# Kernel optimization log

Measured on AMD Instinct MI355X. Metric: run time of the kernel, lower is better.

The kernel has to match this reference:

```python
import jax, jax.numpy as jnp
import numpy as np
from jax import lax

EPS = 1e-5
TAU = 2.0
THR = 1.0

@jax.custom_vjp
def spike_fn(x):
    # torch.heaviside(x, 1.0): 1 where x >= 0, else 0
    return (x >= 0).astype(x.dtype)

def _spike_fwd(x):
    return spike_fn(x), x

def _spike_bwd(x, g):
    alpha = 4.0
    s = jax.nn.sigmoid(alpha * x)
    return (g * (1.0 - s) * s * alpha,)

spike_fn.defvjp(_spike_fwd, _spike_bwd)

def lif(x):
    # sequential membrane recurrence over dim 0 (time)
    def step(v, xt):
        v = v + (xt - v) / TAU
        s = spike_fn(v - THR)
        v = (1.0 - lax.stop_gradient(s)) * v
        return v, s
    _, spikes = lax.scan(step, jnp.zeros_like(x[0]), x)
    return spikes

def bn(x, p):
    # eval-mode BatchNorm2d; p = [weight, bias, mean, var], each [C]
    w, b, m, v = p
    inv = w / jnp.sqrt(v + EPS)
    return (x - m[None, :, None, None]) * inv[None, :, None, None] + b[None, :, None, None]

def bn_and_pad(x, p):
    # BN then pad 1 pixel on all sides with the BN-of-zero value
    w, b, m, v = p
    y = bn(x, p)
    pad_val = b - m * w / jnp.sqrt(v + EPS)  # [C]
    y = jnp.pad(y, ((0, 0), (0, 0), (1, 1), (1, 1)))
    pv = pad_val[None, :, None]  # broadcasts over batch and spatial
    y = y.at[:, :, 0, :].set(pv)
    y = y.at[:, :, -1, :].set(pv)
    y = y.at[:, :, :, 0].set(pv)
    y = y.at[:, :, :, -1].set(pv)
    return y

def branch(x, w1, dw, pw, bn3):
    # RepConv: 1x1 -> BNAndPad(1) -> depthwise3x3(valid) -> 1x1 -> BN, then outer BN
    C = x.shape[1]
    y = jnp.einsum('oc,bchw->bohw', w1, x)
    y = bn_and_pad(y, bn3[0])
    y = lax.conv_general_dilated(y, dw[:, None, :, :], (1, 1), 'VALID',
                                 dimension_numbers=('NCHW', 'OIHW', 'NCHW'),
                                 feature_group_count=C)
    y = jnp.einsum('oc,bchw->bohw', pw, y)
    y = bn(y, bn3[1])
    y = bn(y, bn3[2])
    return y

def _to_heads(t, B, N, h, d):
    # [B,C,H,W] -> [B,h,N,d]
    return t.reshape(B, h * d, N).transpose(0, 2, 1).reshape(B, N, h, d).transpose(0, 2, 1, 3)

def forward(x, q_w1, q_dw, q_pw, q_bn, k_w1, k_dw, k_pw, k_bn,
            v_w1, v_dw, v_pw, v_bn, p_w1, p_dw, p_pw, p_bn,
            num_heads=8):
    B, C, H, W = x.shape
    N = H * W
    h = num_heads
    d = C // h
    scale = float(d) ** -0.5

    xs = lif(x)
    q = lif(branch(xs, q_w1, q_dw, q_pw, q_bn))
    k = lif(branch(xs, k_w1, k_dw, k_pw, k_bn))
    v = lif(branch(xs, v_w1, v_dw, v_pw, v_bn))

    q = _to_heads(q, B, N, h, d)
    k = _to_heads(k, B, N, h, d)
    v = _to_heads(v, B, N, h, d)

    kv = jnp.einsum('bhnd,bhne->bhde', k, v)          # [B,h,d,d]
    o = jnp.einsum('bhnd,bhde->bhne', q, kv) * scale  # [B,h,N,d]
    o = o.transpose(0, 1, 3, 2).reshape(B, C, N)       # [B,C,N]
    o = lif(o)
    o = o.reshape(B, C, H, W)
    o = branch(o, p_w1, p_dw, p_pw, p_bn)
    return o.reshape(B, C, H, W)

def setup_inputs() -> dict:
    key = jax.random.key(0)
    ks = jax.random.split(key, 20)
    B, C, H, W = 8, 256, 64, 64
    s1 = 1.0 / np.sqrt(C)

    def make_bn(k):
        k1, k2, k3, k4 = jax.random.split(k, 4)
        w = 1.0 + 0.1 * jax.random.normal(k1, (3, C), jnp.float32)
        b = 0.1 * jax.random.normal(k2, (3, C), jnp.float32)
        m = 0.1 * jax.random.normal(k3, (3, C), jnp.float32)
        var = jax.random.uniform(k4, (3, C), jnp.float32, 0.5, 1.5)
        return jnp.stack([w, b, m, var], axis=1)  # [3,4,C]

    inp = {'x': jax.random.normal(ks[0], (B, C, H, W), jnp.float32)}
    for i, p in enumerate(['q', 'k', 'v', 'p']):
        kk = jax.random.split(ks[1 + i], 4)
        inp[p + '_w1'] = jax.random.normal(kk[0], (C, C), jnp.float32) * s1
        inp[p + '_dw'] = jax.random.normal(kk[1], (C, 3, 3), jnp.float32) * 0.3
        inp[p + '_pw'] = jax.random.normal(kk[2], (C, C), jnp.float32) * s1
        inp[p + '_bn'] = make_bn(kk[3])
    return inp

def reference(x, q_w1, q_dw, q_pw, q_bn, k_w1, k_dw, k_pw, k_bn,
              v_w1, v_dw, v_pw, v_bn, p_w1, p_dw, p_pw, p_bn):
    return forward(x, q_w1, q_dw, q_pw, q_bn, k_w1, k_dw, k_pw, k_bn,
                   v_w1, v_dw, v_pw, v_bn, p_w1, p_dw, p_pw, p_bn)
```

## Files before the change

### kernel.cpp

```cpp
#include <hip/hip_runtime.h>
#include <hip/hip_bf16.h>
#include <math.h>

#define T_ 8
#define C_ 256
#define N_ 4096
#define CN_ (C_ * N_)
#define EPSB 1e-5f

typedef unsigned long long u64;
typedef unsigned int u32;
typedef short bf16x8 __attribute__((ext_vector_type(8)));
typedef float f32x4 __attribute__((ext_vector_type(4)));

static __device__ __forceinline__ unsigned short f2bf(float f) {
    __hip_bfloat16 h = __float2bfloat16(f);
    return *(unsigned short*)&h;
}
static __device__ __forceinline__ float bf2f(unsigned short u) {
    u32 x = (u32)u << 16;
    return *(float*)&x;
}


__global__ __launch_bounds__(256) void lif_u8(const float* __restrict__ X,
                                              unsigned char* __restrict__ S) {
    int idx = blockIdx.x * 256 + threadIdx.x;
    float v = 0.f;
#pragma unroll
    for (int t = 0; t < T_; t++) {
        float xt = X[(size_t)t * CN_ + idx];
        v = v + (xt - v) / 2.0f;
        unsigned char s = (v - 1.0f >= 0.f) ? 1 : 0;
        S[(size_t)t * CN_ + idx] = s;
        if (s) v = 0.f;
    }
}

struct LArgs {
    const float* F[3];
    unsigned char* sq;
    u64* kbp;
    u64* vbp;
};
__global__ __launch_bounds__(256) void lif3(LArgs a) {
    int br = blockIdx.y;
    int idx = blockIdx.x * 256 + threadIdx.x;
    const float* X = a.F[br];
    int lane = threadIdx.x & 63;
    u64* BP = (br == 1) ? a.kbp : a.vbp;
    float v = 0.f;
#pragma unroll
    for (int t = 0; t < T_; t++) {
        float xt = X[(size_t)t * CN_ + idx];
        v = v + (xt - v) / 2.0f;
        int s = (v - 1.0f >= 0.f) ? 1 : 0;
        if (br == 0) {
            a.sq[(size_t)t * CN_ + idx] = (unsigned char)s;
        } else {
            u64 mask = __ballot(s);
            if (lane == 0) BP[((size_t)t * CN_ + idx) >> 6] = mask;
        }
        if (s) v = 0.f;
    }
}

struct WPtrs { const float* w[8]; };
__global__ __launch_bounds__(256) void split_w(WPtrs p, unsigned short* __restrict__ out) {
    int mat = blockIdx.y;
    int idx = blockIdx.x * 256 + threadIdx.x;
    int m = idx >> 8, k = idx & 255;
    float w = p.w[mat][idx];
    unsigned short h1 = f2bf(w);
    float f1 = bf2f(h1);
    unsigned short h2 = f2bf(w - f1);
    unsigned short h3 = f2bf(w - f1 - bf2f(h2));
    int lane = ((k >> 3) & 3) * 16 + (m & 15);
    size_t pos = ((size_t)(((m >> 4) * 8 + (k >> 5)) * 64 + lane)) * 8 + (k & 7);
    size_t base = (size_t)mat * 3 * 65536;
    out[base + pos] = h1;
    out[base + 65536 + pos] = h2;
    out[base + 2 * 65536 + pos] = h3;
}

__global__ __launch_bounds__(256) void trans_s(const unsigned char* __restrict__ S,
                                               unsigned short* __restrict__ ST) {
    int t = blockIdx.y;
    int nb = blockIdx.x * 32;
    const unsigned char* St = S + (size_t)t * CN_;
    __shared__ u32 L[32][257];
    int tid = threadIdx.x;
    int nof = (tid & 7) * 4;
    int kbase = tid >> 3;
#pragma unroll
    for (int it = 0; it < 8; it++) {
        int k = kbase + it * 32;
        uchar4 sv = *(const uchar4*)&St[(size_t)k * N_ + nb + nof];
        L[nof + 0][k] = sv.x ? 0x3F80u : 0u;
        L[nof + 1][k] = sv.y ? 0x3F80u : 0u;
        L[nof + 2][k] = sv.z ? 0x3F80u : 0u;
        L[nof + 3][k] = sv.w ? 0x3F80u : 0u;
    }
    __syncthreads();
    int n = tid & 31, k32 = tid >> 5;
    int n16 = (nb + n) >> 4;
    int lrow = n & 15;
    unsigned short* outt = ST + (size_t)t * CN_;
#pragma unroll
    for (int quad = 0; quad < 4; quad++) {
        bf16x8 bs;
#pragma unroll
        for (int j = 0; j < 8; j++)
            bs[j] = (short)(L[n][k32 * 32 + quad * 8 + j] & 0xffffu);
        *(bf16x8*)&outt[((size_t)(n16 * 8 + k32)) * 512 + (quad * 16 + lrow) * 8] = bs;
    }
}

static __device__ __forceinline__ void dw_body(const float* __restrict__ Yt,
                                               const float* __restrict__ dw,
                                               const float* __restrict__ bnp,
                                               unsigned short* __restrict__ Bh,
                                               unsigned short* __restrict__ Bl,
                                               int y0, int cg, int tid) {
    int c0 = cg * 8;
    __shared__ float L[8][6][68];
    __shared__ float invs[8], bs_[8], ms_[8], pads_[8];

    if (tid < 8) {
        int c = c0 + tid;
        float w = bnp[c], b = bnp[256 + c], m = bnp[512 + c], var = bnp[768 + c];
        float sq = sqrtf(var + EPSB);
        invs[tid] = w / sq;
        bs_[tid] = b;
        ms_[tid] = m;
        pads_[tid] = b - (m * w) / sq;
    }
    __syncthreads();

    for (int i = tid; i < 8 * 6 * 66; i += 256) {
        int c = i / 396;
        int rem = i - c * 396;
        int row = rem / 66, col = rem - row * 66;
        int gy = y0 - 1 + row, gx = col - 1;
        float val;
        if (gy < 0 || gy > 63 || gx < 0 || gx > 63) val = pads_[c];
        else val = (Yt[(size_t)(c0 + c) * N_ + gy * 64 + gx] - ms_[c]) * invs[c] + bs_[c];
        L[c][row][col] = val;
    }
    __syncthreads();

    int x = tid & 63, ry = tid >> 6;
    int n = (y0 + ry) * 64 + x;

    bf16x8 hi, lo;
#pragma unroll
    for (int j = 0; j < 8; j++) {
        const float* dwc = dw + (c0 + j) * 9;
        float a = 0.f;
#pragma unroll
        for (int dy = 0; dy < 3; dy++)
#pragma unroll
            for (int dx = 0; dx < 3; dx++)
                a += dwc[dy * 3 + dx] * L[j][ry + dy][x + dx];
        unsigned short h = f2bf(a);
        hi[j] = (short)h;
        lo[j] = (short)f2bf(a - bf2f(h));
    }
    size_t pos = ((size_t)((n >> 4) * 8 + (cg >> 2))) * 512 +
                 (size_t)(((cg & 3) * 16 + (n & 15)) * 8);
    *(bf16x8*)&Bh[pos] = hi;
    *(bf16x8*)&Bl[pos] = lo;
}

__global__ __launch_bounds__(256) void dw_bn_split(const float* __restrict__ Yin,
                                                   const float* __restrict__ dw,
                                                   const float* __restrict__ bnp,
                                                   unsigned short* __restrict__ BhT,
                                                   unsigned short* __restrict__ BlT) {
    int t = blockIdx.z;
    dw_body(Yin + (size_t)t * CN_, dw, bnp,
            BhT + (size_t)t * CN_, BlT + (size_t)t * CN_,
            blockIdx.x * 4, blockIdx.y, threadIdx.x);
}

struct DArgs {
    const float* F[3];
    const float* dw[3];
    const float* bn[3];
    unsigned short* Ph[3];
    unsigned short* Pl[3];
};
__global__ __launch_bounds__(256) void dw3(DArgs a) {
    int br = blockIdx.z >> 3, t = blockIdx.z & 7;
    dw_body(a.F[br] + (size_t)t * CN_, a.dw[br], a.bn[br],
            a.Ph[br] + (size_t)t * CN_, a.Pl[br] + (size_t)t * CN_,
            blockIdx.x * 4, blockIdx.y, threadIdx.x);
}

static __device__ __forceinline__ void gemm_s_core(const unsigned short* __restrict__ Wsp,
                                                   const unsigned short* __restrict__ Bt,
                                                   float* __restrict__ Yt,
                                                   int bx, int by, int tid) {
    int l = tid & 63, wave = tid >> 6;
    int wm = wave >> 1, wn = wave & 1;
    int lcol = l & 15, quad = l >> 4;

    f32x4 acc[4][4];
#pragma unroll
    for (int i = 0; i < 4; i++)
#pragma unroll
        for (int j = 0; j < 4; j++) acc[i][j] = (f32x4){0.f, 0.f, 0.f, 0.f};

#pragma unroll 2
    for (int k32 = 0; k32 < 8; k32++) {
        bf16x8 bfr[4];
#pragma unroll
        for (int nt = 0; nt < 4; nt++)
            bfr[nt] = *(const bf16x8*)&Bt[((size_t)((bx * 8 + wn * 4 + nt) * 8 + k32)) * 512 + l * 8];
#pragma unroll
        for (int s = 0; s < 3; s++) {
            const unsigned short* Ws = Wsp + (size_t)s * 65536;
#pragma unroll
            for (int mt = 0; mt < 4; mt++) {
                bf16x8 afr = *(const bf16x8*)&Ws[((size_t)((by * 8 + wm * 4 + mt) * 8 + k32)) * 512 + l * 8];
#pragma unroll
                for (int nt = 0; nt < 4; nt++)
                    acc[mt][nt] = __builtin_amdgcn_mfma_f32_16x16x32_bf16(
                        afr, bfr[nt], acc[mt][nt], 0, 0, 0);
            }
        }
    }

    int m0 = by * 128, n0 = bx * 128;
#pragma unroll
    for (int mt = 0; mt < 4; mt++)
#pragma unroll
        for (int i = 0; i < 4; i++) {
            int row = m0 + wm * 64 + mt * 16 + quad * 4 + i;
            float* yr = &Yt[(size_t)row * N_ + n0 + wn * 64 + lcol];
#pragma unroll
            for (int nt = 0; nt < 4; nt++) yr[nt * 16] = acc[mt][nt][i];
        }
}

static __device__ __forceinline__ void gemm_f_core(const unsigned short* __restrict__ Wsp,
                                                   const unsigned short* __restrict__ Bht,
                                                   const unsigned short* __restrict__ Blt,
                                                   float* __restrict__ Yt,
                                                   const float* __restrict__ bnp,
                                                   int bx, int by, int tid) {
    int l = tid & 63, wave = tid >> 6;
    int wm = wave >> 1, wn = wave & 1;
    int lcol = l & 15, quad = l >> 4;

    f32x4 acc[4][4];
#pragma unroll
    for (int i = 0; i < 4; i++)
#pragma unroll
        for (int j = 0; j < 4; j++) acc[i][j] = (f32x4){0.f, 0.f, 0.f, 0.f};

#pragma unroll 2
    for (int k32 = 0; k32 < 8; k32++) {
        bf16x8 bh[4], bl[4];
#pragma unroll
        for (int nt = 0; nt < 4; nt++) {
            size_t bpos = ((size_t)((bx * 8 + wn * 4 + nt) * 8 + k32)) * 512 + l * 8;
            bh[nt] = *(const bf16x8*)&Bht[bpos];
            bl[nt] = *(const bf16x8*)&Blt[bpos];
        }
#pragma unroll
        for (int s = 0; s < 3; s++) {
            const unsigned short* Ws = Wsp + (size_t)s * 65536;
#pragma unroll
            for (int mt = 0; mt < 4; mt++) {
                bf16x8 afr = *(const bf16x8*)&Ws[((size_t)((by * 8 + wm * 4 + mt) * 8 + k32)) * 512 + l * 8];
#pragma unroll
                for (int nt = 0; nt < 4; nt++)
                    acc[mt][nt] = __builtin_amdgcn_mfma_f32_16x16x32_bf16(
                        afr, bh[nt], acc[mt][nt], 0, 0, 0);
                if (s < 2) {
#pragma unroll
                    for (int nt = 0; nt < 4; nt++)
                        acc[mt][nt] = __builtin_amdgcn_mfma_f32_16x16x32_bf16(
                            afr, bl[nt], acc[mt][nt], 0, 0, 0);
                }
            }
        }
    }

    int m0 = by * 128, n0 = bx * 128;
#pragma unroll
    for (int mt = 0; mt < 4; mt++)
#pragma unroll
        for (int i = 0; i < 4; i++) {
            int row = m0 + wm * 64 + mt * 16 + quad * 4 + i;
            float i1 = bnp[1024 + row] / sqrtf(bnp[1024 + 768 + row] + EPSB);
            float b1 = bnp[1024 + 256 + row], m1 = bnp[1024 + 512 + row];
            float i2 = bnp[2048 + row] / sqrtf(bnp[2048 + 768 + row] + EPSB);
            float b2 = bnp[2048 + 256 + row], m2 = bnp[2048 + 512 + row];
            float* yr = &Yt[(size_t)row * N_ + n0 + wn * 64 + lcol];
#pragma unroll
            for (int nt = 0; nt < 4; nt++)
                yr[nt * 16] = ((acc[mt][nt][i] - m1) * i1 + b1 - m2) * i2 + b2;
        }
}

__global__ __launch_bounds__(256) void gemm_s2(const unsigned short* __restrict__ Wsp,
                                               const unsigned short* __restrict__ ST,
                                               float* __restrict__ Y) {
    int t = blockIdx.z;
    gemm_s_core(Wsp, ST + (size_t)t * CN_, Y + (size_t)t * CN_,
                blockIdx.x, blockIdx.y, threadIdx.x);
}
__global__ __launch_bounds__(256) void gemm_f2(const unsigned short* __restrict__ Wsp,
                                               const unsigned short* __restrict__ BhT,
                                               const unsigned short* __restrict__ BlT,
                                               float* __restrict__ Y,
                                               const float* __restrict__ bnp) {
    int t = blockIdx.z;
    gemm_f_core(Wsp, BhT + (size_t)t * CN_, BlT + (size_t)t * CN_,
                Y + (size_t)t * CN_, bnp, blockIdx.x, blockIdx.y, threadIdx.x);
}

struct GSArgs { const unsigned short* W[3]; const unsigned short* ST; float* F[3]; };
__global__ __launch_bounds__(256) void gemm_s3(GSArgs a) {
    int t = blockIdx.z;
    int br = blockIdx.y >> 1, byl = blockIdx.y & 1;
    gemm_s_core(a.W[br], a.ST + (size_t)t * CN_, a.F[br] + (size_t)t * CN_,
                blockIdx.x, byl, threadIdx.x);
}
struct GFArgs {
    const unsigned short* W[3];
    const unsigned short* Ph[3];
    const unsigned short* Pl[3];
    float* F[3];
    const float* bn[3];
};
__global__ __launch_bounds__(256) void gemm_f3(GFArgs a) {
    int t = blockIdx.z;
    int br = blockIdx.y >> 1, byl = blockIdx.y & 1;
    gemm_f_core(a.W[br], a.Ph[br] + (size_t)t * CN_, a.Pl[br] + (size_t)t * CN_,
                a.F[br] + (size_t)t * CN_, a.bn[br], blockIdx.x, byl, threadIdx.x);
}

__global__ __launch_bounds__(1024) void attn_kv_bp(const u64* __restrict__ Kbp,
                                                   const u64* __restrict__ Vbp,
                                                   float* __restrict__ kvbuf) {
    int th = blockIdx.x;
    int t = th >> 3, h = th & 7;
    const u64* kb = Kbp + ((size_t)t * C_ + h * 32) * 64;
    const u64* vb = Vbp + ((size_t)t * C_ + h * 32) * 64;
    __shared__ u64 ks[32][65];
    __shared__ u64 vs[32][65];
    int tid = threadIdx.x;
    {
        int r = tid >> 5, w2 = (tid & 31) * 2;
        ks[r][w2] = kb[r * 64 + w2];     ks[r][w2 + 1] = kb[r * 64 + w2 + 1];
        vs[r][w2] = vb[r * 64 + w2];     vs[r][w2 + 1] = vb[r * 64 + w2 + 1];
    }
    __syncthreads();
    int d = tid >> 5, e = tid & 31;
    int cnt = 0;
#pragma unroll
    for (int w = 0; w < 64; w++)
        cnt += __popcll(ks[d][w] & vs[e][w]);
    kvbuf[(size_t)th * 1024 + d * 32 + e] = (float)cnt;
}

__global__ __launch_bounds__(256) void attn_o_u8(const unsigned char* __restrict__ q,
                                                 const float* __restrict__ kvbuf,
                                                 float* __restrict__ o) {
    int t = blockIdx.z, h = blockIdx.y;
    int n = blockIdx.x * 1024 + threadIdx.x * 4;
    __shared__ float kvs[1024];
    const float* kv = kvbuf + (size_t)(t * 8 + h) * 1024;
    for (int i = threadIdx.x; i < 1024; i += 256) kvs[i] = kv[i];
    __syncthreads();
    const unsigned char* qb = q + (size_t)t * CN_ + (size_t)h * 32 * N_ + n;
    float* ob = o + (size_t)t * CN_ + (size_t)h * 32 * N_ + n;
    const float scale = 0.17677669529663687f;
#pragma unroll
    for (int eg = 0; eg < 2; eg++) {
        float acc[16][4];
#pragma unroll
        for (int e = 0; e < 16; e++)
#pragma unroll
            for (int j = 0; j < 4; j++) acc[e][j] = 0.f;
        for (int d = 0; d < 32; d++) {
            uchar4 qu = *(const uchar4*)(&qb[(size_t)d * N_]);
            float4 qv = {(float)qu.x, (float)qu.y, (float)qu.z, (float)qu.w};
#pragma unroll
            for (int e = 0; e < 16; e++) {
                float kvv = kvs[d * 32 + eg * 16 + e];
                acc[e][0] += qv.x * kvv;
                acc[e][1] += qv.y * kvv;
                acc[e][2] += qv.z * kvv;
                acc[e][3] += qv.w * kvv;
            }
        }
#pragma unroll
        for (int e = 0; e < 16; e++) {
            float4 ov = {acc[e][0] * scale, acc[e][1] * scale,
                         acc[e][2] * scale, acc[e][3] * scale};
            *(float4*)(&ob[(size_t)(eg * 16 + e) * N_]) = ov;
        }
    }
}

extern "C" void kernel_launch(void* const* d_in, const int* in_sizes, int n_in,
                              void* d_out, int out_size, void* d_ws, size_t ws_size,
                              hipStream_t stream) {
    const float* x = (const float*)d_in[0];
    const float* q_w1 = (const float*)d_in[1];
    const float* q_dw = (const float*)d_in[2];
    const float* q_pw = (const float*)d_in[3];
    const float* q_bn = (const float*)d_in[4];
    const float* k_w1 = (const float*)d_in[5];
    const float* k_dw = (const float*)d_in[6];
    const float* k_pw = (const float*)d_in[7];
    const float* k_bn = (const float*)d_in[8];
    const float* v_w1 = (const float*)d_in[9];
    const float* v_dw = (const float*)d_in[10];
    const float* v_pw = (const float*)d_in[11];
    const float* v_bn = (const float*)d_in[12];
    const float* p_w1 = (const float*)d_in[13];
    const float* p_dw = (const float*)d_in[14];
    const float* p_pw = (const float*)d_in[15];
    const float* p_bn = (const float*)d_in[16];

    const size_t SZ = (size_t)T_ * CN_;
    float* out = (float*)d_out;
    float* F0 = (float*)d_ws;
    float* F1 = F0 + SZ;
    float* F2 = F1 + SZ;
    float* P0 = F2 + SZ;
    float* P1 = P0 + SZ;
    float* P2 = P1 + SZ;
    float* bufKV = P2 + SZ;
    unsigned char* xs = (unsigned char*)(bufKV + 65536);
    unsigned char* sq = xs + SZ;
    u64* kbp = (u64*)(sq + SZ);
    u64* vbp = kbp + (SZ >> 6);
    unsigned short* wspA = (unsigned short*)(vbp + (SZ >> 6));
    unsigned short* ST = wspA + 8 * 3 * 65536;

    unsigned short* P0h = (unsigned short*)P0; unsigned short* P0l = P0h + SZ;
    unsigned short* P1h = (unsigned short*)P1; unsigned short* P1l = P1h + SZ;
    unsigned short* P2h = (unsigned short*)P2; unsigned short* P2l = P2h + SZ;

    dim3 gLif(CN_ / 256), bLif(256);
    dim3 gTr(N_ / 32, T_), bTr(256);

    WPtrs wp;
    wp.w[0] = q_w1; wp.w[1] = q_pw; wp.w[2] = k_w1; wp.w[3] = k_pw;
    wp.w[4] = v_w1; wp.w[5] = v_pw; wp.w[6] = p_w1; wp.w[7] = p_pw;
    split_w<<<dim3(256, 8), dim3(256), 0, stream>>>(wp, wspA);
    const size_t WS3 = 3 * 65536;

    lif_u8<<<gLif, bLif, 0, stream>>>(x, xs);
    trans_s<<<gTr, bTr, 0, stream>>>(xs, ST);

    GSArgs gs;
    gs.W[0] = wspA + 0 * WS3; gs.W[1] = wspA + 2 * WS3; gs.W[2] = wspA + 4 * WS3;
    gs.ST = ST; gs.F[0] = F0; gs.F[1] = F1; gs.F[2] = F2;
    gemm_s3<<<dim3(N_ / 128, 6, T_), dim3(256), 0, stream>>>(gs);

    DArgs da;
    da.F[0] = F0; da.F[1] = F1; da.F[2] = F2;
    da.dw[0] = q_dw; da.dw[1] = k_dw; da.dw[2] = v_dw;
    da.bn[0] = q_bn; da.bn[1] = k_bn; da.bn[2] = v_bn;
    da.Ph[0] = P0h; da.Ph[1] = P1h; da.Ph[2] = P2h;
    da.Pl[0] = P0l; da.Pl[1] = P1l; da.Pl[2] = P2l;
    dw3<<<dim3(16, 32, 3 * T_), dim3(256), 0, stream>>>(da);

    GFArgs gf;
    gf.W[0] = wspA + 1 * WS3; gf.W[1] = wspA + 3 * WS3; gf.W[2] = wspA + 5 * WS3;
    gf.Ph[0] = P0h; gf.Ph[1] = P1h; gf.Ph[2] = P2h;
    gf.Pl[0] = P0l; gf.Pl[1] = P1l; gf.Pl[2] = P2l;
    gf.F[0] = F0; gf.F[1] = F1; gf.F[2] = F2;
    gf.bn[0] = q_bn; gf.bn[1] = k_bn; gf.bn[2] = v_bn;
    gemm_f3<<<dim3(N_ / 128, 6, T_), dim3(256), 0, stream>>>(gf);

    LArgs la;
    la.F[0] = F0; la.F[1] = F1; la.F[2] = F2;
    la.sq = sq; la.kbp = kbp; la.vbp = vbp;
    lif3<<<dim3(CN_ / 256, 3), dim3(256), 0, stream>>>(la);

    attn_kv_bp<<<dim3(64), dim3(1024), 0, stream>>>(kbp, vbp, bufKV);
    attn_o_u8<<<dim3(4, 8, 8), dim3(256), 0, stream>>>(sq, bufKV, F0);
    lif_u8<<<gLif, bLif, 0, stream>>>(F0, xs);
    trans_s<<<gTr, bTr, 0, stream>>>(xs, ST);

    gemm_s2<<<dim3(N_ / 128, C_ / 128, T_), dim3(256), 0, stream>>>(wspA + 6 * WS3, ST, out);
    dw_bn_split<<<dim3(16, 32, T_), dim3(256), 0, stream>>>(out, p_dw, p_bn, P0h, P0l);
    gemm_f2<<<dim3(N_ / 128, C_ / 128, T_), dim3(256), 0, stream>>>(wspA + 7 * WS3, P0h, P0l, out, p_bn);
}
```

Measured before the change: 442.7 us.

## Fuse LIF with spike transpose, and attention output with LIF

The input LIF now writes bf16 MFMA-fragment spikes directly, so the separate uint8 spike buffer and transpose kernel are gone. The attention-output kernel now loops over time per head, keeps membrane state in registers, and emits bf16 fragment spikes directly. This removes the fp32 attention-output buffer, the second LIF pass and a transpose, saving global memory traffic and several launches. In exchange the new kernels synchronise at every timestep, and attn_olif launches far fewer blocks and reads q with byte-sized loads, which may lower occupancy and memory efficiency.

```diff
diff --git a/kernel.cpp b/kernel.cpp
--- a/kernel.cpp
+++ b/kernel.cpp
@@ -23,17 +23,33 @@
 }
 
 
-__global__ __launch_bounds__(256) void lif_u8(const float* __restrict__ X,
-                                              unsigned char* __restrict__ S) {
-    int idx = blockIdx.x * 256 + threadIdx.x;
+__global__ __launch_bounds__(256) void lif_x_frag(const float* __restrict__ X,
+                                                  unsigned short* __restrict__ ST) {
+    int nb = blockIdx.x * 32;
+    int c0 = blockIdx.y * 8;
+    int tid = threadIdx.x;
+    int nj = tid & 31, ci = tid >> 5;
+    size_t base = (size_t)(c0 + ci) * N_ + nb + nj;
+    __shared__ unsigned short Ls[8][34];
+    int k32 = c0 >> 5, quad = (c0 >> 3) & 3;
     float v = 0.f;
 #pragma unroll
     for (int t = 0; t < T_; t++) {
-        float xt = X[(size_t)t * CN_ + idx];
+        float xt = X[(size_t)t * CN_ + base];
         v = v + (xt - v) / 2.0f;
-        unsigned char s = (v - 1.0f >= 0.f) ? 1 : 0;
-        S[(size_t)t * CN_ + idx] = s;
+        int s = (v - 1.0f >= 0.f) ? 1 : 0;
+        Ls[ci][nj] = s ? (unsigned short)0x3F80 : (unsigned short)0;
         if (s) v = 0.f;
+        __syncthreads();
+        if (tid < 32) {
+            int np = nb + tid;
+            bf16x8 bs;
+#pragma unroll
+            for (int j = 0; j < 8; j++) bs[j] = (short)Ls[j][tid];
+            *(bf16x8*)&ST[(size_t)t * CN_ +
+                ((size_t)((np >> 4) * 8 + k32)) * 512 + (quad * 16 + (np & 15)) * 8] = bs;
+        }
+        __syncthreads();
     }
 }
 
@@ -83,39 +99,6 @@
     out[base + 2 * 65536 + pos] = h3;
 }
 
-__global__ __launch_bounds__(256) void trans_s(const unsigned char* __restrict__ S,
-                                               unsigned short* __restrict__ ST) {
-    int t = blockIdx.y;
-    int nb = blockIdx.x * 32;
-    const unsigned char* St = S + (size_t)t * CN_;
-    __shared__ u32 L[32][257];
-    int tid = threadIdx.x;
-    int nof = (tid & 7) * 4;
-    int kbase = tid >> 3;
-#pragma unroll
-    for (int it = 0; it < 8; it++) {
-        int k = kbase + it * 32;
-        uchar4 sv = *(const uchar4*)&St[(size_t)k * N_ + nb + nof];
-        L[nof + 0][k] = sv.x ? 0x3F80u : 0u;
-        L[nof + 1][k] = sv.y ? 0x3F80u : 0u;
-        L[nof + 2][k] = sv.z ? 0x3F80u : 0u;
-        L[nof + 3][k] = sv.w ? 0x3F80u : 0u;
-    }
-    __syncthreads();
-    int n = tid & 31, k32 = tid >> 5;
-    int n16 = (nb + n) >> 4;
-    int lrow = n & 15;
-    unsigned short* outt = ST + (size_t)t * CN_;
-#pragma unroll
-    for (int quad = 0; quad < 4; quad++) {
-        bf16x8 bs;
-#pragma unroll
-        for (int j = 0; j < 8; j++)
-            bs[j] = (short)(L[n][k32 * 32 + quad * 8 + j] & 0xffffu);
-        *(bf16x8*)&outt[((size_t)(n16 * 8 + k32)) * 512 + (quad * 16 + lrow) * 8] = bs;
-    }
-}
-
 static __device__ __forceinline__ void dw_body(const float* __restrict__ Yt,
                                                const float* __restrict__ dw,
                                                const float* __restrict__ bnp,
@@ -367,43 +350,51 @@
     kvbuf[(size_t)th * 1024 + d * 32 + e] = (float)cnt;
 }
 
-__global__ __launch_bounds__(256) void attn_o_u8(const unsigned char* __restrict__ q,
+__global__ __launch_bounds__(256) void attn_olif(const unsigned char* __restrict__ q,
                                                  const float* __restrict__ kvbuf,
-                                                 float* __restrict__ o) {
-    int t = blockIdx.z, h = blockIdx.y;
-    int n = blockIdx.x * 1024 + threadIdx.x * 4;
+                                                 unsigned short* __restrict__ ST) {
+    int h = blockIdx.y;
+    int nb = blockIdx.x * 128;
+    int tid = threadIdx.x;
+    int nj = tid & 127, eh = tid >> 7;
+    int n = nb + nj;
     __shared__ float kvs[1024];
-    const float* kv = kvbuf + (size_t)(t * 8 + h) * 1024;
-    for (int i = threadIdx.x; i < 1024; i += 256) kvs[i] = kv[i];
-    __syncthreads();
-    const unsigned char* qb = q + (size_t)t * CN_ + (size_t)h * 32 * N_ + n;
-    float* ob = o + (size_t)t * CN_ + (size_t)h * 32 * N_ + n;
     const float scale = 0.17677669529663687f;
-#pragma unroll
-    for (int eg = 0; eg < 2; eg++) {
-        float acc[16][4];
-#pragma unroll
-        for (int e = 0; e < 16; e++)
-#pragma unroll
-            for (int j = 0; j < 4; j++) acc[e][j] = 0.f;
+    float v[16];
+#pragma unroll
+    for (int e = 0; e < 16; e++) v[e] = 0.f;
+    size_t posbase = ((size_t)((n >> 4) * 8 + h)) * 512 + (size_t)(n & 15) * 8;
+    int quad0 = 2 * eh;
+#pragma unroll
+    for (int t = 0; t < T_; t++) {
+        for (int i = tid; i < 1024; i += 256)
+            kvs[i] = kvbuf[(size_t)(t * 8 + h) * 1024 + i];
+        __syncthreads();
+        float acc[16];
+#pragma unroll
+        for (int e = 0; e < 16; e++) acc[e] = 0.f;
+        const unsigned char* qb = q + (size_t)t * CN_ + (size_t)(h * 32) * N_ + n;
+#pragma unroll 4
         for (int d = 0; d < 32; d++) {
-            uchar4 qu = *(const uchar4*)(&qb[(size_t)d * N_]);
-            float4 qv = {(float)qu.x, (float)qu.y, (float)qu.z, (float)qu.w};
-#pragma unroll
-            for (int e = 0; e < 16; e++) {
-                float kvv = kvs[d * 32 + eg * 16 + e];
-                acc[e][0] += qv.x * kvv;
-                acc[e][1] += qv.y * kvv;
-                acc[e][2] += qv.z * kvv;
-                acc[e][3] += qv.w * kvv;
-            }
-        }
+            float qd = (float)qb[(size_t)d * N_];
+#pragma unroll
+            for (int e = 0; e < 16; e++)
+                acc[e] += qd * kvs[d * 32 + eh * 16 + e];
+        }
+        bf16x8 w0, w1;
 #pragma unroll
         for (int e = 0; e < 16; e++) {
-            float4 ov = {acc[e][0] * scale, acc[e][1] * scale,
-                         acc[e][2] * scale, acc[e][3] * scale};
-            *(float4*)(&ob[(size_t)(eg * 16 + e) * N_]) = ov;
-        }
+            float o = acc[e] * scale;
+            v[e] = v[e] + (o - v[e]) / 2.0f;
+            int s = (v[e] - 1.0f >= 0.f) ? 1 : 0;
+            short bits = s ? (short)0x3F80 : (short)0;
+            if (e < 8) w0[e] = bits; else w1[e - 8] = bits;
+            if (s) v[e] = 0.f;
+        }
+        unsigned short* Stt = ST + (size_t)t * CN_;
+        *(bf16x8*)&Stt[posbase + (size_t)(quad0 * 16) * 8] = w0;
+        *(bf16x8*)&Stt[posbase + (size_t)((quad0 + 1) * 16) * 8] = w1;
+        __syncthreads();
     }
 }
 
@@ -448,17 +439,13 @@
     unsigned short* P1h = (unsigned short*)P1; unsigned short* P1l = P1h + SZ;
     unsigned short* P2h = (unsigned short*)P2; unsigned short* P2l = P2h + SZ;
 
-    dim3 gLif(CN_ / 256), bLif(256);
-    dim3 gTr(N_ / 32, T_), bTr(256);
-
     WPtrs wp;
     wp.w[0] = q_w1; wp.w[1] = q_pw; wp.w[2] = k_w1; wp.w[3] = k_pw;
     wp.w[4] = v_w1; wp.w[5] = v_pw; wp.w[6] = p_w1; wp.w[7] = p_pw;
     split_w<<<dim3(256, 8), dim3(256), 0, stream>>>(wp, wspA);
     const size_t WS3 = 3 * 65536;
 
-    lif_u8<<<gLif, bLif, 0, stream>>>(x, xs);
-    trans_s<<<gTr, bTr, 0, stream>>>(xs, ST);
+    lif_x_frag<<<dim3(N_ / 32, C_ / 8), dim3(256), 0, stream>>>(x, ST);
 
     GSArgs gs;
     gs.W[0] = wspA + 0 * WS3; gs.W[1] = wspA + 2 * WS3; gs.W[2] = wspA + 4 * WS3;
@@ -487,9 +474,7 @@
     lif3<<<dim3(CN_ / 256, 3), dim3(256), 0, stream>>>(la);
 
     attn_kv_bp<<<dim3(64), dim3(1024), 0, stream>>>(kbp, vbp, bufKV);
-    attn_o_u8<<<dim3(4, 8, 8), dim3(256), 0, stream>>>(sq, bufKV, F0);
-    lif_u8<<<gLif, bLif, 0, stream>>>(F0, xs);
-    trans_s<<<gTr, bTr, 0, stream>>>(xs, ST);
+    attn_olif<<<dim3(N_ / 128, 8), dim3(256), 0, stream>>>(sq, bufKV, ST);
 
     gemm_s2<<<dim3(N_ / 128, C_ / 128, T_), dim3(256), 0, stream>>>(wspA + 6 * WS3, ST, out);
     dw_bn_split<<<dim3(16, 32, T_), dim3(256), 0, stream>>>(out, p_dw, p_bn, P0h, P0l);
```

Result: no change. 446.2 us (+0.8%).
